# Kernel tuning notes

Measured on AMD Instinct MI355X. Metric: run time of the kernel, lower is better.

Reference implementation:

```python
import jax, jax.numpy as jnp
import numpy as np

WS = 8            # current window
PRETRAIN = 8      # pretrain window
HEADS = 8
C = 256
UNITS = C // HEADS
SHIFT = WS // 2   # shift_mode=1 -> shift_dir=[1,1], apply_shift True (H,W > WS)
EPS = 1.55e-5
LOG100 = float(np.log(100.0))

# ---- static relative-position index and log-spaced coord table (SwinV2 CPB) ----
_c = np.arange(WS)
_rel_h = _c[:, None] - _c[None, :] + (WS - 1)          # [WS,WS] in [0, 2WS-2]
REL_INDEX = (_rel_h[:, None, :, None] * (2 * WS - 1) + _rel_h[None, :, None, :]).reshape(WS * WS, WS * WS)
_r = np.arange(-(WS - 1), WS, dtype=np.float32)
_t = np.stack(np.meshgrid(_r, _r, indexing='ij'), axis=-1).reshape(-1, 2)  # [(2WS-1)^2, 2]
_t = _t / (PRETRAIN - 1) * 8.0
CPB_TABLE = np.sign(_t) * np.log2(1.0 + np.abs(_t)) / np.log2(8.0)


def _shift_mask(H, W):
    # region labels per Swin shift mask: segments (dim-WS, WS-SHIFT, SHIFT) for shift_dir=+1
    def seg(n):
        s = np.zeros(n, np.int32)
        s[n - WS:n - SHIFT] = 1
        s[n - SHIFT:] = 2
        return s
    img = seg(H)[:, None] * 3 + seg(W)[None, :] + 1      # [H,W]
    img = img.reshape(H // WS, WS, W // WS, WS).transpose(0, 2, 1, 3).reshape(-1, WS * WS)
    d = img[:, :, None] - img[:, None, :]
    return np.where(d == 0, 0.0, -100.0).astype(np.float32)  # [nW, WS^2, WS^2]

SHIFT_MASK = _shift_mask(256, 256)


def _partition(t, H, W):
    # [B,H,W,C] -> [B,nW,heads,WS^2,units]
    B = t.shape[0]
    t = t.reshape(B, H // WS, WS, W // WS, WS, HEADS, UNITS)
    t = t.transpose(0, 1, 3, 5, 2, 4, 6)
    return t.reshape(B, (H // WS) * (W // WS), HEADS, WS * WS, UNITS)


def _reverse(t, H, W):
    B = t.shape[0]
    t = t.reshape(B, H // WS, W // WS, HEADS, WS, WS, UNITS)
    t = t.transpose(0, 1, 4, 2, 5, 3, 6)
    return t.reshape(B, H, W, C)


def _l2n(t):
    return t / jnp.sqrt(jnp.maximum(jnp.sum(t * t, axis=-1, keepdims=True), EPS))


def setup_inputs():
    key = jax.random.key(0)
    ks = jax.random.split(key, 6)
    return {
        'x': jax.random.normal(ks[0], (2, 256, 256, C), jnp.float32),
        'qkv_w': jax.random.normal(ks[1], (C, 3 * C), jnp.float32) * 0.02,
        'q_bias': jnp.zeros((C,), jnp.float32),
        'v_bias': jnp.zeros((C,), jnp.float32),
        'scale': jnp.full((HEADS, 1, 1), np.log(10.0), jnp.float32),
        'cpb_w1': jax.random.normal(ks[2], (2, 512), jnp.float32) * 0.02,
        'cpb_b1': jnp.zeros((512,), jnp.float32),
        'cpb_w2': jax.random.normal(ks[3], (512, HEADS), jnp.float32) * 0.02,
        'proj_w': jax.random.normal(ks[4], (C, C), jnp.float32) * 0.02,
        'proj_b': jnp.zeros((C,), jnp.float32),
    }


def reference(x, qkv_w, q_bias, v_bias, scale, cpb_w1, cpb_b1, cpb_w2, proj_w, proj_b):
    B, H, W, _ = x.shape
    qkv = x @ qkv_w + jnp.concatenate([q_bias, jnp.zeros_like(q_bias), v_bias])
    qkv = jnp.roll(qkv, (-SHIFT, -SHIFT), axis=(1, 2))
    q, k, v = jnp.split(qkv, 3, axis=-1)
    q = _l2n(_partition(q, H, W))          # [B,nW,h,WS^2,u]
    k = _l2n(_partition(k, H, W))
    v = _partition(v, H, W)
    logit_scale = jnp.exp(jnp.minimum(scale, LOG100))  # [h,1,1]
    attn = jnp.einsum('bwhqd,bwhkd->bwhqk', q * logit_scale, k)
    # continuous relative position bias
    cpb = jax.nn.relu(jnp.asarray(CPB_TABLE) @ cpb_w1 + cpb_b1) @ cpb_w2  # [(2WS-1)^2, h]
    bias = 16.0 * jax.nn.sigmoid(cpb[REL_INDEX])                          # [WS^2,WS^2,h]
    bias = bias.transpose(2, 0, 1)                                        # [h,WS^2,WS^2]
    attn = attn + bias[None, None] + jnp.asarray(SHIFT_MASK)[None, :, None]
    attn = jax.nn.softmax(attn, axis=-1)
    out = jnp.einsum('bwhqk,bwhkd->bwhqd', attn, v)
    out = _reverse(out, H, W)
    out = jnp.roll(out, (SHIFT, SHIFT), axis=(1, 2))
    return out @ proj_w + proj_b
```

## Files before the change

kernel.cpp:

```cpp
#include <hip/hip_runtime.h>


typedef _Float16 f16;
typedef _Float16 f16x4 __attribute__((ext_vector_type(4)));
typedef _Float16 f16x8 __attribute__((ext_vector_type(8)));
typedef float f32x4 __attribute__((ext_vector_type(4)));

#define LOG100 4.6051701859880914f
#define EPS_L2 1.55e-5f

__device__ __forceinline__ int seg2(int p) { return (p >= 248) + (p >= 252); }

__global__ __launch_bounds__(512) void k_prep(
    const float* __restrict__ cpb_w1, const float* __restrict__ cpb_b1,
    const float* __restrict__ cpb_w2, const float* __restrict__ qkv_w,
    const float* __restrict__ proj_w,
    float* __restrict__ biasfrag, f16* __restrict__ w_t, f16* __restrict__ p_t)
{
    int tid = threadIdx.x;
    if (blockIdx.x == 0) {
        __shared__ float Lw1[1024];
        __shared__ float Lb1[512];
        __shared__ float Lw2[4096];
        __shared__ float part[450 * 8];
        __shared__ float cpb[225 * 8];
        #pragma unroll
        for (int i = tid; i < 1024; i += 512) Lw1[i] = cpb_w1[i];
        if (tid < 512) Lb1[tid] = cpb_b1[tid];
        #pragma unroll
        for (int i = tid; i < 4096; i += 512) Lw2[i] = cpb_w2[i];
        __syncthreads();
        {
            int e = tid >> 1, half = tid & 1;
            if (e < 225) {
                int a = e / 15, b2 = e % 15;
                float xa = (float)(a - 7) * (8.0f / 7.0f);
                float xb = (float)(b2 - 7) * (8.0f / 7.0f);
                float t0 = (xa < 0.f ? -1.f : 1.f) * log2f(1.0f + fabsf(xa)) * (1.0f / 3.0f);
                float t1 = (xb < 0.f ? -1.f : 1.f) * log2f(1.0f + fabsf(xb)) * (1.0f / 3.0f);
                float acc[8] = {0.f, 0.f, 0.f, 0.f, 0.f, 0.f, 0.f, 0.f};
                int j0 = half << 8;
                #pragma unroll 4
                for (int j = j0; j < j0 + 256; ++j) {
                    float hh = fmaxf(t0 * Lw1[j] + t1 * Lw1[512 + j] + Lb1[j], 0.0f);
                    #pragma unroll
                    for (int h = 0; h < 8; ++h) acc[h] += hh * Lw2[j * 8 + h];
                }
                #pragma unroll
                for (int h = 0; h < 8; ++h) part[tid * 8 + h] = acc[h];
            }
        }
        __syncthreads();
        if (tid < 225) {
            #pragma unroll
            for (int h = 0; h < 8; ++h)
                cpb[tid * 8 + h] = part[tid * 16 + h] + part[tid * 16 + 8 + h];
        }
        __syncthreads();
        for (int f = tid; f < 32768; f += 512) {
            int r = f & 3, lane = (f >> 2) & 63, nt = (f >> 8) & 3, mt = (f >> 10) & 3, h = (f >> 12) & 7;
            int k = mt * 16 + ((lane >> 4) << 2) + r;
            int q = nt * 16 + (lane & 15);
            int idx = ((q >> 3) - (k >> 3) + 7) * 15 + ((q & 7) - (k & 7) + 7);
            float c = cpb[idx * 8 + h];
            biasfrag[f] = 16.0f / (1.0f + expf(-c));
        }
    } else {
        int base = (blockIdx.x - 1) * 512 + tid;
        const int stride = 128 * 512;
        for (int i = base; i < 768 * 256; i += stride) {
            int n = i >> 8, k = i & 255;
            w_t[i] = (f16)qkv_w[k * 768 + n];
        }
        for (int i = base; i < 256 * 256; i += stride) {
            int n = i >> 8, k = i & 255;
            p_t[i] = (f16)proj_w[k * 256 + n];
        }
    }
}

__global__ __launch_bounds__(512) void k_fused(
    const float* __restrict__ x, const f16* __restrict__ w_t,
    const float* __restrict__ q_bias, const float* __restrict__ v_bias,
    const float* __restrict__ scale, const float* __restrict__ biasfrag,
    const f16* __restrict__ p_t, const float* __restrict__ proj_b,
    float* __restrict__ out)
{
    __shared__ char L[65536];
    const int tid = threadIdx.x;
    const int lane = tid & 63;
    const int h = tid >> 6;
    const int l15 = lane & 15, g = lane >> 4;
    const int bw = blockIdx.x;
    const int win = bw & 1023, b = bw >> 10;
    const int wh = win >> 5, ww = win & 31;
    char* wb = L + 32768 + (h << 12);
    char* vtr = L + (h << 12);
    const f32x4 fz = {0.f, 0.f, 0.f, 0.f};
    const bool boundary = (wh == 31) || (ww == 31);

    {
        int pos = tid >> 3, tc = tid & 7;
        int i2 = ((wh << 3) + (pos >> 3) + 4) & 255;
        int j2 = ((ww << 3) + (pos & 7) + 4) & 255;
        const float* xr = x + ((((long)b << 8) + i2) * 256 + j2) * 256;
        int swz = (pos & 7) << 4;
        #pragma unroll
        for (int rep = 0; rep < 4; ++rep) {
            int ch = rep * 64 + tc * 8;
            float4 v0 = *reinterpret_cast<const float4*>(xr + ch);
            float4 v1 = *reinterpret_cast<const float4*>(xr + ch + 4);
            f16x8 hv = { (f16)v0.x, (f16)v0.y, (f16)v0.z, (f16)v0.w,
                         (f16)v1.x, (f16)v1.y, (f16)v1.z, (f16)v1.w };
            *reinterpret_cast<f16x8*>(L + ((pos * 512 + ch * 2) ^ swz)) = hv;
        }
    }
    __syncthreads();

    f16x8 qa[4], kb[4];

    auto qk_pass = [&](int p, float ls, bool addb, f16x8 frag[4]) {
        f32x4 acc[2][4];
        #pragma unroll
        for (int i = 0; i < 2; ++i)
            #pragma unroll
            for (int j = 0; j < 4; ++j) acc[i][j] = fz;
        #pragma unroll
        for (int ks = 0; ks < 8; ++ks) {
            f16x8 xf[4], wf[2];
            #pragma unroll
            for (int mt = 0; mt < 4; ++mt) {
                int row = mt * 16 + l15;
                xf[mt] = *reinterpret_cast<const f16x8*>(
                    L + ((row * 512 + ks * 64 + g * 16) ^ ((row & 7) << 4)));
            }
            #pragma unroll
            for (int ct = 0; ct < 2; ++ct)
                wf[ct] = *reinterpret_cast<const f16x8*>(
                    w_t + ((p << 8) + (h << 5) + ct * 16 + l15) * 256 + ks * 32 + g * 8);
            #pragma unroll
            for (int ct = 0; ct < 2; ++ct)
                #pragma unroll
                for (int mt = 0; mt < 4; ++mt)
                    acc[ct][mt] = __builtin_amdgcn_mfma_f32_16x16x32_f16(wf[ct], xf[mt], acc[ct][mt], 0, 0, 0);
        }
        float qb0[4], qb1[4];
        #pragma unroll
        for (int r = 0; r < 4; ++r) {
            qb0[r] = addb ? q_bias[(h << 5) + (g << 2) + r] : 0.f;
            qb1[r] = addb ? q_bias[(h << 5) + 16 + (g << 2) + r] : 0.f;
        }
        #pragma unroll
        for (int nt = 0; nt < 4; ++nt) {
            int pix = nt * 16 + l15;
            float t0[4], t1[4], s2 = 0.f;
            #pragma unroll
            for (int r = 0; r < 4; ++r) {
                t0[r] = acc[0][nt][r] + qb0[r];
                t1[r] = acc[1][nt][r] + qb1[r];
                s2 += t0[r] * t0[r] + t1[r] * t1[r];
            }
            s2 += __shfl_xor(s2, 16); s2 += __shfl_xor(s2, 32);
            float iv = ls / sqrtf(fmaxf(s2, EPS_L2));
            int sw = (pix & 7) << 4;
            f16x4 p0 = { (f16)(t0[0] * iv), (f16)(t0[1] * iv), (f16)(t0[2] * iv), (f16)(t0[3] * iv) };
            f16x4 p1 = { (f16)(t1[0] * iv), (f16)(t1[1] * iv), (f16)(t1[2] * iv), (f16)(t1[3] * iv) };
            *reinterpret_cast<f16x4*>(wb + ((pix * 64 + (g << 3)) ^ sw)) = p0;
            *reinterpret_cast<f16x4*>(wb + ((pix * 64 + 32 + (g << 3)) ^ sw)) = p1;
        }
        #pragma unroll
        for (int nt = 0; nt < 4; ++nt)
            frag[nt] = *reinterpret_cast<const f16x8*>(
                wb + (((nt * 16 + l15) * 64 + g * 16) ^ ((l15 & 7) << 4)));
    };

    qk_pass(0, __expf(fminf(scale[h], LOG100)), true, qa);
    __builtin_amdgcn_sched_barrier(0);
    qk_pass(1, 1.0f, false, kb);
    __builtin_amdgcn_sched_barrier(0);

    {
        f32x4 av[4][2];
        #pragma unroll
        for (int mt = 0; mt < 4; ++mt) { av[mt][0] = fz; av[mt][1] = fz; }
        #pragma unroll
        for (int ks = 0; ks < 8; ++ks) {
            f16x8 xf[4], wv[2];
            #pragma unroll
            for (int mt = 0; mt < 4; ++mt) {
                int row = mt * 16 + l15;
                xf[mt] = *reinterpret_cast<const f16x8*>(
                    L + ((row * 512 + ks * 64 + g * 16) ^ ((row & 7) << 4)));
            }
            #pragma unroll
            for (int nt = 0; nt < 2; ++nt)
                wv[nt] = *reinterpret_cast<const f16x8*>(
                    w_t + (512 + (h << 5) + nt * 16 + l15) * 256 + ks * 32 + g * 8);
            #pragma unroll
            for (int mt = 0; mt < 4; ++mt)
                #pragma unroll
                for (int nt = 0; nt < 2; ++nt)
                    av[mt][nt] = __builtin_amdgcn_mfma_f32_16x16x32_f16(xf[mt], wv[nt], av[mt][nt], 0, 0, 0);
        }
        __syncthreads();
        float b0 = v_bias[(h << 5) + l15], b1 = v_bias[(h << 5) + 16 + l15];
        #pragma unroll
        for (int mt = 0; mt < 4; ++mt)
            #pragma unroll
            for (int nt = 0; nt < 2; ++nt) {
                float bsel = nt ? b1 : b0;
                f32x4 avv = av[mt][nt];
                f16x4 pk = { (f16)(avv[0] + bsel), (f16)(avv[1] + bsel),
                             (f16)(avv[2] + bsel), (f16)(avv[3] + bsel) };
                int u = nt * 16 + l15;
                int pix0 = mt * 16 + (g << 2);
                *reinterpret_cast<f16x4*>(vtr + ((u * 128 + pix0 * 2) ^ ((u & 7) << 4))) = pk;
            }
    }
    __builtin_amdgcn_sched_barrier(0);

    f16x4 oh[4][2];
    #pragma unroll
    for (int c = 0; c < 2; ++c) {
        #pragma unroll
        for (int n2 = 0; n2 < 2; ++n2) {
            const int nt = c * 2 + n2;
            const int qrow = nt * 16 + l15;
            f32x4 st[4];
            #pragma unroll
            for (int mt = 0; mt < 4; ++mt)
                st[mt] = __builtin_amdgcn_mfma_f32_16x16x32_f16(kb[mt], qa[nt], fz, 0, 0, 0);
            #pragma unroll
            for (int mt = 0; mt < 4; ++mt)
                st[mt] += *reinterpret_cast<const f32x4*>(
                    biasfrag + ((((h * 4 + mt) * 4 + nt) * 64 + lane) << 2));
            if (boundary) {
                int lq = seg2((wh << 3) + (qrow >> 3)) * 3 + seg2((ww << 3) + (qrow & 7));
                #pragma unroll
                for (int mt = 0; mt < 4; ++mt)
                    #pragma unroll
                    for (int r = 0; r < 4; ++r) {
                        int k = mt * 16 + (g << 2) + r;
                        int lk = seg2((wh << 3) + (k >> 3)) * 3 + seg2((ww << 3) + (k & 7));
                        if (lq != lk) st[mt][r] -= 100.0f;
                    }
            }
            float mx = st[0][0];
            #pragma unroll
            for (int mt = 0; mt < 4; ++mt)
                #pragma unroll
                for (int r = 0; r < 4; ++r) mx = fmaxf(mx, st[mt][r]);
            mx = fmaxf(mx, __shfl_xor(mx, 16));
            mx = fmaxf(mx, __shfl_xor(mx, 32));
            float sm = 0.f;
            #pragma unroll
            for (int mt = 0; mt < 4; ++mt)
                #pragma unroll
                for (int r = 0; r < 4; ++r) {
                    float e = __expf(st[mt][r] - mx);
                    st[mt][r] = e;
                    sm += e;
                }
            sm += __shfl_xor(sm, 16);
            sm += __shfl_xor(sm, 32);
            float inv = 1.0f / sm;
            int sw = (qrow & 7) << 4;
            int rowb = (qrow & 31) * 128;
            #pragma unroll
            for (int mt = 0; mt < 4; ++mt) {
                f16x4 pk = { (f16)(st[mt][0] * inv), (f16)(st[mt][1] * inv),
                             (f16)(st[mt][2] * inv), (f16)(st[mt][3] * inv) };
                *reinterpret_cast<f16x4*>(wb + ((rowb + mt * 32 + (g << 3)) ^ sw)) = pk;
            }
        }
        #pragma unroll
        for (int m2 = 0; m2 < 2; ++m2) {
            const int mt = c * 2 + m2;
            int row = m2 * 16 + l15;
            int swz = (row & 7) << 4;
            f16x8 pa0 = *reinterpret_cast<const f16x8*>(wb + ((row * 128 + g * 16) ^ swz));
            f16x8 pa1 = *reinterpret_cast<const f16x8*>(wb + ((row * 128 + 64 + g * 16) ^ swz));
            #pragma unroll
            for (int nt = 0; nt < 2; ++nt) {
                f16x8 vf0 = *reinterpret_cast<const f16x8*>(
                    vtr + (((nt * 16 + l15) * 128 + g * 16) ^ ((l15 & 7) << 4)));
                f16x8 vf1 = *reinterpret_cast<const f16x8*>(
                    vtr + (((nt * 16 + l15) * 128 + 64 + g * 16) ^ ((l15 & 7) << 4)));
                f32x4 t = __builtin_amdgcn_mfma_f32_16x16x32_f16(pa0, vf0, fz, 0, 0, 0);
                t = __builtin_amdgcn_mfma_f32_16x16x32_f16(pa1, vf1, t, 0, 0, 0);
                oh[mt][nt] = f16x4{ (f16)t[0], (f16)t[1], (f16)t[2], (f16)t[3] };
            }
        }
    }
    __builtin_amdgcn_sched_barrier(0);

    __syncthreads();
    #pragma unroll
    for (int mt = 0; mt < 4; ++mt)
        #pragma unroll
        for (int r = 0; r < 4; ++r) {
            int q = mt * 16 + (g << 2) + r;
            #pragma unroll
            for (int nt = 0; nt < 2; ++nt) {
                int ch = (h << 5) + nt * 16 + l15;
                *reinterpret_cast<f16*>(L + ((q * 512 + ch * 2) ^ ((q & 7) << 4))) =
                    oh[mt][nt][r];
            }
        }
    __syncthreads();

    const int c0 = h << 5;
    f32x4 pc[4][2];
    #pragma unroll
    for (int mt = 0; mt < 4; ++mt) { pc[mt][0] = fz; pc[mt][1] = fz; }
    #pragma unroll
    for (int ks = 0; ks < 8; ++ks) {
        f16x8 a[4], bfr[2];
        #pragma unroll
        for (int mt = 0; mt < 4; ++mt) {
            int q = mt * 16 + l15;
            a[mt] = *reinterpret_cast<const f16x8*>(
                L + ((q * 512 + ks * 64 + g * 16) ^ ((q & 7) << 4)));
        }
        #pragma unroll
        for (int nt = 0; nt < 2; ++nt)
            bfr[nt] = *reinterpret_cast<const f16x8*>(
                p_t + (c0 + nt * 16 + l15) * 256 + ks * 32 + g * 8);
        #pragma unroll
        for (int mt = 0; mt < 4; ++mt)
            #pragma unroll
            for (int nt = 0; nt < 2; ++nt)
                pc[mt][nt] = __builtin_amdgcn_mfma_f32_16x16x32_f16(a[mt], bfr[nt], pc[mt][nt], 0, 0, 0);
    }
    float pb0 = proj_b[c0 + l15], pb1 = proj_b[c0 + 16 + l15];
    #pragma unroll
    for (int mt = 0; mt < 4; ++mt)
        #pragma unroll
        for (int r = 0; r < 4; ++r) {
            int q = mt * 16 + (g << 2) + r;
            int i = ((wh << 3) + (q >> 3) + 4) & 255;
            int j = ((ww << 3) + (q & 7) + 4) & 255;
            long addr = (((long)b * 256 + i) * 256 + j) * 256;
            out[addr + c0 + l15]      = pc[mt][0][r] + pb0;
            out[addr + c0 + 16 + l15] = pc[mt][1][r] + pb1;
        }
}

extern "C" void kernel_launch(void* const* d_in, const int* in_sizes, int n_in,
                              void* d_out, int out_size, void* d_ws, size_t ws_size,
                              hipStream_t stream) {
    const float* x      = (const float*)d_in[0];
    const float* qkv_w  = (const float*)d_in[1];
    const float* q_bias = (const float*)d_in[2];
    const float* v_bias = (const float*)d_in[3];
    const float* scale  = (const float*)d_in[4];
    const float* cpb_w1 = (const float*)d_in[5];
    const float* cpb_b1 = (const float*)d_in[6];
    const float* cpb_w2 = (const float*)d_in[7];
    const float* proj_w = (const float*)d_in[8];
    const float* proj_b = (const float*)d_in[9];
    float* out = (float*)d_out;

    char* ws = (char*)d_ws;
    float* biasfrag = (float*)(ws);
    f16* w_t  = (f16*)(ws + 131072);
    f16* p_t  = (f16*)(ws + 524288);

    hipLaunchKernelGGL(k_prep, dim3(129), dim3(512), 0, stream,
                       cpb_w1, cpb_b1, cpb_w2, qkv_w, proj_w, biasfrag, w_t, p_t);
    hipLaunchKernelGGL(k_fused, dim3(2048), dim3(512), 0, stream,
                       x, w_t, q_bias, v_bias, scale, biasfrag, p_t, proj_b, out);
}
```

Before: 242.2 us.

## Split fused kernel into half-head attention blocks plus separate projection kernel

The fused attention kernel now runs two 256-thread blocks per window, each covering four heads with 48KB of LDS, and writes the fp16 attention output to a global buffer. A new k_proj kernel reloads that buffer per window and applies the output projection. The aim is more resident blocks per CU and smaller per-block LDS and register pressure. The cost is a global round trip of the attention output, the x tile and its staging being repeated for each half, and an extra kernel launch.

```diff
diff --git a/kernel.cpp b/kernel.cpp
--- a/kernel.cpp
+++ b/kernel.cpp
@@ -79,35 +79,37 @@
     }
 }
 
-__global__ __launch_bounds__(512) void k_fused(
+__global__ __launch_bounds__(256) void k_fused(
     const float* __restrict__ x, const f16* __restrict__ w_t,
     const float* __restrict__ q_bias, const float* __restrict__ v_bias,
     const float* __restrict__ scale, const float* __restrict__ biasfrag,
-    const f16* __restrict__ p_t, const float* __restrict__ proj_b,
-    float* __restrict__ out)
+    f16* __restrict__ obuf)
 {
-    __shared__ char L[65536];
+    __shared__ char L[49152];
     const int tid = threadIdx.x;
     const int lane = tid & 63;
-    const int h = tid >> 6;
+    const int wv = tid >> 6;
     const int l15 = lane & 15, g = lane >> 4;
-    const int bw = blockIdx.x;
+    const int bh = blockIdx.x;
+    const int bw = bh >> 1, half = bh & 1;
     const int win = bw & 1023, b = bw >> 10;
     const int wh = win >> 5, ww = win & 31;
-    char* wb = L + 32768 + (h << 12);
-    char* vtr = L + (h << 12);
+    const int h = half * 4 + wv;
+    char* wb = L + 32768 + (wv << 12);
+    char* vtr = L + (wv << 12);
+    char* ot = L + 16384;
     const f32x4 fz = {0.f, 0.f, 0.f, 0.f};
     const bool boundary = (wh == 31) || (ww == 31);
 
     {
-        int pos = tid >> 3, tc = tid & 7;
+        int pos = tid >> 2, tc = tid & 3;
         int i2 = ((wh << 3) + (pos >> 3) + 4) & 255;
         int j2 = ((ww << 3) + (pos & 7) + 4) & 255;
         const float* xr = x + ((((long)b << 8) + i2) * 256 + j2) * 256;
         int swz = (pos & 7) << 4;
         #pragma unroll
-        for (int rep = 0; rep < 4; ++rep) {
-            int ch = rep * 64 + tc * 8;
+        for (int rep = 0; rep < 8; ++rep) {
+            int ch = rep * 32 + tc * 8;
             float4 v0 = *reinterpret_cast<const float4*>(xr + ch);
             float4 v1 = *reinterpret_cast<const float4*>(xr + ch + 4);
             f16x8 hv = { (f16)v0.x, (f16)v0.y, (f16)v0.z, (f16)v0.w,
@@ -185,7 +187,7 @@
         for (int mt = 0; mt < 4; ++mt) { av[mt][0] = fz; av[mt][1] = fz; }
         #pragma unroll
         for (int ks = 0; ks < 8; ++ks) {
-            f16x8 xf[4], wv[2];
+            f16x8 xf[4], wvf[2];
             #pragma unroll
             for (int mt = 0; mt < 4; ++mt) {
                 int row = mt * 16 + l15;
@@ -194,13 +196,13 @@
             }
             #pragma unroll
             for (int nt = 0; nt < 2; ++nt)
-                wv[nt] = *reinterpret_cast<const f16x8*>(
+                wvf[nt] = *reinterpret_cast<const f16x8*>(
                     w_t + (512 + (h << 5) + nt * 16 + l15) * 256 + ks * 32 + g * 8);
             #pragma unroll
             for (int mt = 0; mt < 4; ++mt)
                 #pragma unroll
                 for (int nt = 0; nt < 2; ++nt)
-                    av[mt][nt] = __builtin_amdgcn_mfma_f32_16x16x32_f16(xf[mt], wv[nt], av[mt][nt], 0, 0, 0);
+                    av[mt][nt] = __builtin_amdgcn_mfma_f32_16x16x32_f16(xf[mt], wvf[nt], av[mt][nt], 0, 0, 0);
         }
         __syncthreads();
         float b0 = v_bias[(h << 5) + l15], b1 = v_bias[(h << 5) + 16 + l15];
@@ -219,7 +221,6 @@
     }
     __builtin_amdgcn_sched_barrier(0);
 
-    f16x4 oh[4][2];
     #pragma unroll
     for (int c = 0; c < 2; ++c) {
         #pragma unroll
@@ -288,25 +289,56 @@
                     vtr + (((nt * 16 + l15) * 128 + 64 + g * 16) ^ ((l15 & 7) << 4)));
                 f32x4 t = __builtin_amdgcn_mfma_f32_16x16x32_f16(pa0, vf0, fz, 0, 0, 0);
                 t = __builtin_amdgcn_mfma_f32_16x16x32_f16(pa1, vf1, t, 0, 0, 0);
-                oh[mt][nt] = f16x4{ (f16)t[0], (f16)t[1], (f16)t[2], (f16)t[3] };
-            }
-        }
-    }
-    __builtin_amdgcn_sched_barrier(0);
-
+                #pragma unroll
+                for (int r = 0; r < 4; ++r) {
+                    int q = mt * 16 + (g << 2) + r;
+                    int ch2 = (wv << 5) + nt * 16 + l15;
+                    *reinterpret_cast<f16*>(ot + ((q * 256 + ch2 * 2) ^ ((q & 7) << 4))) =
+                        (f16)t[r];
+                }
+            }
+        }
+    }
     __syncthreads();
-    #pragma unroll
-    for (int mt = 0; mt < 4; ++mt)
-        #pragma unroll
-        for (int r = 0; r < 4; ++r) {
-            int q = mt * 16 + (g << 2) + r;
-            #pragma unroll
-            for (int nt = 0; nt < 2; ++nt) {
-                int ch = (h << 5) + nt * 16 + l15;
-                *reinterpret_cast<f16*>(L + ((q * 512 + ch * 2) ^ ((q & 7) << 4))) =
-                    oh[mt][nt][r];
-            }
-        }
+
+    {
+        int r2 = tid >> 2, seg = tid & 3;
+        long dst = ((long)bw * 64 + r2) * 256 + half * 128 + seg * 32;
+        int sw = (r2 & 7) << 4;
+        #pragma unroll
+        for (int i = 0; i < 4; ++i) {
+            f16x8 vv = *reinterpret_cast<const f16x8*>(
+                ot + ((r2 * 256 + seg * 64 + i * 16) ^ sw));
+            *reinterpret_cast<f16x8*>(obuf + dst + i * 8) = vv;
+        }
+    }
+}
+
+__global__ __launch_bounds__(512) void k_proj(
+    const f16* __restrict__ obuf, const f16* __restrict__ p_t,
+    const float* __restrict__ proj_b, float* __restrict__ out)
+{
+    __shared__ char L[32768];
+    const int tid = threadIdx.x;
+    const int lane = tid & 63;
+    const int h = tid >> 6;
+    const int l15 = lane & 15, g = lane >> 4;
+    const int bw = blockIdx.x;
+    const int win = bw & 1023, b = bw >> 10;
+    const int wh = win >> 5, ww = win & 31;
+    const f32x4 fz = {0.f, 0.f, 0.f, 0.f};
+
+    {
+        int row = tid >> 3, tc = tid & 7;
+        const f16* src = obuf + ((long)bw * 64 + row) * 256;
+        int sw = (row & 7) << 4;
+        #pragma unroll
+        for (int rep = 0; rep < 4; ++rep) {
+            int ch = rep * 64 + tc * 8;
+            f16x8 vv = *reinterpret_cast<const f16x8*>(src + ch);
+            *reinterpret_cast<f16x8*>(L + ((row * 512 + ch * 2) ^ sw)) = vv;
+        }
+    }
     __syncthreads();
 
     const int c0 = h << 5;
@@ -365,9 +397,12 @@
     float* biasfrag = (float*)(ws);
     f16* w_t  = (f16*)(ws + 131072);
     f16* p_t  = (f16*)(ws + 524288);
+    f16* obuf = (f16*)(ws + (1u << 20));
 
     hipLaunchKernelGGL(k_prep, dim3(129), dim3(512), 0, stream,
                        cpb_w1, cpb_b1, cpb_w2, qkv_w, proj_w, biasfrag, w_t, p_t);
-    hipLaunchKernelGGL(k_fused, dim3(2048), dim3(512), 0, stream,
-                       x, w_t, q_bias, v_bias, scale, biasfrag, p_t, proj_b, out);
+    hipLaunchKernelGGL(k_fused, dim3(4096), dim3(256), 0, stream,
+                       x, w_t, q_bias, v_bias, scale, biasfrag, obuf);
+    hipLaunchKernelGGL(k_proj, dim3(2048), dim3(512), 0, stream,
+                       obuf, p_t, proj_b, out);
 }
```

New measurement: 258.4 us. +6.7%, slower.
